# Optimization experiments

Measured on AMD Instinct MI355X. Metric: run time of the kernel, lower is better.

Reference implementation:

```python
import jax, jax.numpy as jnp
import numpy as np

BZ, IN_DIM, STATE_DIM, OUT_DIM, L = 16, 512, 512, 512, 2048
INIT_SCALE = 0.5


def setup_inputs() -> dict:
    key = jax.random.key(0)
    k_u, k_a, k_b, k_c = jax.random.split(key, 4)
    u = jax.random.normal(k_u, (BZ, IN_DIM, L), dtype=jnp.float32)
    A_unconstrained = jax.random.normal(k_a, (STATE_DIM,), dtype=jnp.float32) * 0.1
    B = jax.random.normal(k_b, (STATE_DIM, IN_DIM), dtype=jnp.float32) * INIT_SCALE / np.sqrt(IN_DIM)
    C = jax.random.normal(k_c, (OUT_DIM, STATE_DIM), dtype=jnp.float32) * INIT_SCALE / np.sqrt(STATE_DIM)
    D = jnp.zeros((OUT_DIM, IN_DIM), dtype=jnp.float32)
    h0 = jnp.zeros((STATE_DIM,), dtype=jnp.float32)
    return {"u": u, "A_unconstrained": A_unconstrained, "B": B, "C": C, "D": D, "h0": h0}


def reference(u, A_unconstrained, B, C, D, h0):
    # u: (Bz, input_dim, L)
    Bz = u.shape[0]
    A_diag = -jax.nn.softplus(A_unconstrained)  # (S,)
    # Time-invariant input projection, batched over all timesteps: (L, Bz, S)
    Bu = jnp.einsum('bil,si->lbs', u, B)

    state0 = jnp.broadcast_to(h0[None, :], (Bz, h0.shape[0]))

    def step(state, bu_t):
        x_t = state * A_diag[None, :] + bu_t  # (Bz, S)
        return x_t, x_t

    _, xs = jax.lax.scan(step, state0, Bu)  # xs: (L, Bz, S)

    # Output projection: y_t = C x_t + D u_t  -> (Bz, out, L)
    Y = jnp.einsum('lbs,os->bol', xs, C) + jnp.einsum('bil,oi->bol', u, D)
    return Y
```

## Files before the change

kernel.cpp:

```cpp
#include <hip/hip_runtime.h>
#include <math.h>

typedef __bf16 bf16;
typedef __bf16 bf16x2 __attribute__((ext_vector_type(2)));
typedef __bf16 bf16x4 __attribute__((ext_vector_type(4)));
typedef __bf16 bf16x8 __attribute__((ext_vector_type(8)));
typedef float  f32x4  __attribute__((ext_vector_type(4)));

#define BZd 16
#define INd 512
#define Sd  512
#define Od  512
#define Ld  2048
#define CLd 128
#define NCd (Ld / CLd)

__global__ __launch_bounds__(256) void prep_all(const float* __restrict__ B,
                                                const float* __restrict__ C,
                                                const float* __restrict__ D,
                                                const float* __restrict__ Au,
                                                bf16* __restrict__ Bb, bf16* __restrict__ Cb,
                                                bf16* __restrict__ Db, float* __restrict__ A_diag,
                                                int* __restrict__ dflag) {
    int bid = blockIdx.x;
    if (bid == 768) {
        #pragma unroll
        for (int r = 0; r < 2; ++r) {
            int ss = threadIdx.x + r * 256;
            float x = Au[ss];
            float sp = fmaxf(x, 0.0f) + log1pf(expf(-fabsf(x)));
            A_diag[ss] = -sp;
        }
        return;
    }
    int which = bid >> 8, lb = bid & 255;
    const float* src = which == 0 ? B : (which == 1 ? C : D);
    bf16* dst = which == 0 ? Bb : (which == 1 ? Cb : Db);
    int i = lb * 256 + threadIdx.x;
    float4 v = *(const float4*)&src[(size_t)i * 4];
    bf16x4 o = { (bf16)v.x, (bf16)v.y, (bf16)v.z, (bf16)v.w };
    *(bf16x4*)&dst[(size_t)i * 4] = o;
    if (which == 2) {
        bool nz = (v.x != 0.f) | (v.y != 0.f) | (v.z != 0.f) | (v.w != 0.f);
        unsigned long long bl = __ballot(nz);
        if (bl && ((threadIdx.x & 63) == 0)) atomicOr(dflag, 1);
    }
}

__global__ __launch_bounds__(256) void transp_u(const float* __restrict__ u,
                                                bf16* __restrict__ ut) {
    __shared__ bf16 t[64][73];
    int b = blockIdx.z, i0 = blockIdx.y * 64, l0 = blockIdx.x * 64;
    int tid = threadIdx.x, tx = tid & 15, ty = tid >> 4;
    const float* ub = u + ((size_t)b * INd + i0) * Ld + l0;
    #pragma unroll
    for (int r = 0; r < 4; ++r) {
        int il = r * 16 + ty;
        float4 v = *(const float4*)&ub[(size_t)il * Ld + tx * 4];
        t[il][tx * 4 + 0] = (bf16)v.x;
        t[il][tx * 4 + 1] = (bf16)v.y;
        t[il][tx * 4 + 2] = (bf16)v.z;
        t[il][tx * 4 + 3] = (bf16)v.w;
    }
    __syncthreads();
    bf16* uo = ut + ((size_t)b * Ld + l0) * INd + i0;
    #pragma unroll
    for (int it = 0; it < 2; ++it) {
        int q = it * 256 + tid;
        int lr = q >> 3;
        int ic = (q & 7) * 8;
        bf16x8 o;
        #pragma unroll
        for (int e = 0; e < 8; ++e) o[e] = t[ic + e][lr];
        *(bf16x8*)&uo[(size_t)lr * INd + ic] = o;
    }
}

template<bool OBF16>
__global__ __launch_bounds__(512, 2) void gemm8p(
    const bf16* __restrict__ A0, size_t aBS0,
    const bf16* __restrict__ B0, size_t bBS0,
    const bf16* __restrict__ A1, size_t aBS1,
    const bf16* __restrict__ B1, size_t bBS1,
    const int* __restrict__ dfp,
    void* __restrict__ OutV, size_t oBS, int ldOut,
    int NX, int NY)
{
    __shared__ bf16 lds[4 * 16384];
    const int tid = threadIdx.x;
    const int lane = tid & 63, w = tid >> 6;

    int nwg = gridDim.x, bid = blockIdx.x;
    int cpx = nwg >> 3;
    int swz = (bid & 7) * cpx + (bid >> 3);
    int pb = NX * NY;
    int b  = swz / pb;
    int r0 = swz - b * pb;
    int by = r0 / NX;
    int bx = r0 - by * NX;

    const int wm = w >> 2, wn = w & 3;
    const int fr = lane & 15, g = lane >> 4;

    int extra = dfp ? *dfp : 0;
    const int NT = extra ? 16 : 8;
    const int NU = 2 * NT;

    const bf16* Ab0 = A0 + (size_t)b * aBS0 + (size_t)(by * 256) * 512;
    const bf16* Bb0 = B0 + (size_t)b * bBS0 + (size_t)(bx * 256) * 512;
    const bf16* Ab1 = A1 + (size_t)b * aBS1 + (size_t)(by * 256) * 512;
    const bf16* Bb1 = B1 + (size_t)b * bBS1 + (size_t)(bx * 256) * 512;

    f32x4 acc[8][4];
    #pragma unroll
    for (int i = 0; i < 8; ++i)
        #pragma unroll
        for (int j = 0; j < 4; ++j)
            acc[i][j] = (f32x4){0.f, 0.f, 0.f, 0.f};

    auto stage_part = [&](int U, int isB) {
        int T = U >> 1, kh = U & 1;
        const bf16* Mb = isB ? (T >= 8 ? Bb1 : Bb0) : (T >= 8 ? Ab1 : Ab0);
        int kbase = ((T & 7) << 6) + (kh << 5);
        int slot = U & 3;
        #pragma unroll
        for (int rblk = 0; rblk < 2; ++rblk) {
            int row = rblk * 128 + (tid >> 2);
            int pos = tid & 3;
            int cs = pos ^ ((row & 3) ^ ((row >> 2) & 3));
            __builtin_amdgcn_global_load_lds(
                (const __attribute__((address_space(1))) void*)(Mb + (size_t)row * 512 + kbase + cs * 8),
                (__attribute__((address_space(3))) void*)&lds[slot * 16384 + isB * 8192 + (rblk * 128 + w * 16) * 32],
                16, 0, 0);
        }
    };

    stage_part(0, 0); stage_part(0, 1);
    stage_part(1, 0); stage_part(1, 1);
    stage_part(2, 0); stage_part(2, 1);

    bf16x8 av[4], bv[4];
    for (int U = 0; U < NU; ++U) {
        int ahead = NU - 1 - U;
        if (ahead >= 2)      { asm volatile("s_waitcnt vmcnt(8)" ::: "memory"); }
        else if (ahead == 1) { asm volatile("s_waitcnt vmcnt(4)" ::: "memory"); }
        else                 { asm volatile("s_waitcnt vmcnt(0)" ::: "memory"); }
        __builtin_amdgcn_sched_barrier(0);
        __builtin_amdgcn_s_barrier();
        __builtin_amdgcn_sched_barrier(0);

        const bf16* Ls = &lds[(U & 3) * 16384];
        #pragma unroll
        for (int mf = 0; mf < 2; ++mf) {
            if (mf == 1) {
                __builtin_amdgcn_sched_barrier(0);
                __builtin_amdgcn_s_barrier();
                __builtin_amdgcn_sched_barrier(0);
            }
            if (mf == 0) {
                #pragma unroll
                for (int j = 0; j < 4; ++j) {
                    int R = wn * 64 + j * 16 + fr;
                    int pos = g ^ ((R & 3) ^ ((R >> 2) & 3));
                    bv[j] = *(const bf16x8*)&Ls[8192 + R * 32 + pos * 8];
                }
            }
            #pragma unroll
            for (int i = 0; i < 4; ++i) {
                int R = wm * 128 + (mf * 4 + i) * 16 + fr;
                int pos = g ^ ((R & 3) ^ ((R >> 2) & 3));
                av[i] = *(const bf16x8*)&Ls[R * 32 + pos * 8];
            }
            if (U + 3 < NU) stage_part(U + 3, mf);
            asm volatile("s_waitcnt lgkmcnt(0)" ::: "memory");
            __builtin_amdgcn_sched_barrier(0);
            __builtin_amdgcn_s_setprio(1);
            #pragma unroll
            for (int i = 0; i < 4; ++i)
                #pragma unroll
                for (int j = 0; j < 4; ++j)
                    acc[mf * 4 + i][j] = __builtin_amdgcn_mfma_f32_16x16x32_bf16(
                        av[i], bv[j], acc[mf * 4 + i][j], 0, 0, 0);
            __builtin_amdgcn_s_setprio(0);
        }
    }

    int m0 = by * 256 + wm * 128 + g * 4;
    int n0 = bx * 256 + wn * 64 + fr;
    if (OBF16) {
        bf16* out = (bf16*)OutV + (size_t)b * oBS;
        #pragma unroll
        for (int i = 0; i < 8; ++i)
            #pragma unroll
            for (int j = 0; j < 4; ++j)
                #pragma unroll
                for (int q = 0; q < 4; ++q)
                    out[(size_t)(m0 + i * 16 + q) * ldOut + n0 + j * 16] = (bf16)acc[i][j][q];
    } else {
        float* out = (float*)OutV + (size_t)b * oBS;
        #pragma unroll
        for (int i = 0; i < 8; ++i)
            #pragma unroll
            for (int j = 0; j < 4; ++j)
                #pragma unroll
                for (int q = 0; q < 4; ++q)
                    out[(size_t)(m0 + i * 16 + q) * ldOut + n0 + j * 16] = acc[i][j][q];
    }
}

__global__ __launch_bounds__(256) void pass_ce2(const bf16* __restrict__ xbuf,
                                                const float* __restrict__ A_diag,
                                                float* __restrict__ ce) {
    int gI = blockIdx.x * 256 + threadIdx.x;
    int sp = gI & 255;
    int c = (gI >> 8) & (NCd - 1);
    int b = gI >> 12;
    int s = sp * 2;
    float a0 = A_diag[s], a1 = A_diag[s + 1];
    const bf16* p = xbuf + ((size_t)b * Ld + (size_t)c * CLd) * Sd + s;
    float x0 = 0.f, x1 = 0.f;
    #pragma unroll 4
    for (int j = 0; j < CLd; ++j) {
        bf16x2 v = *(const bf16x2*)&p[(size_t)j * Sd];
        x0 = fmaf(a0, x0, (float)v[0]);
        x1 = fmaf(a1, x1, (float)v[1]);
    }
    float2 o = { x0, x1 };
    *(float2*)&ce[((size_t)b * NCd + c) * Sd + s] = o;
}

__global__ __launch_bounds__(256) void pass_scan2(bf16* __restrict__ xbuf,
                                                  const float* __restrict__ A_diag,
                                                  const float* __restrict__ ce,
                                                  const float* __restrict__ h0) {
    int gI = blockIdx.x * 256 + threadIdx.x;
    int sp = gI & 255;
    int c = (gI >> 8) & (NCd - 1);
    int b = gI >> 12;
    int s = sp * 2;
    float a0 = A_diag[s], a1 = A_diag[s + 1];
    float acl0 = a0, acl1 = a1;
    #pragma unroll
    for (int i = 0; i < 7; ++i) { acl0 *= acl0; acl1 *= acl1; }
    float x0 = h0[s], x1 = h0[s + 1];
    for (int cp = 0; cp < NCd; ++cp) {
        if (cp >= c) break;
        float2 e = *(const float2*)&ce[((size_t)b * NCd + cp) * Sd + s];
        x0 = fmaf(acl0, x0, e.x);
        x1 = fmaf(acl1, x1, e.y);
    }
    bf16* p = xbuf + ((size_t)b * Ld + (size_t)c * CLd) * Sd + s;
    #pragma unroll 4
    for (int j = 0; j < CLd; ++j) {
        bf16x2 v = *(const bf16x2*)&p[(size_t)j * Sd];
        x0 = fmaf(a0, x0, (float)v[0]);
        x1 = fmaf(a1, x1, (float)v[1]);
        bf16x2 o = { (bf16)x0, (bf16)x1 };
        *(bf16x2*)&p[(size_t)j * Sd] = o;
    }
}

extern "C" void kernel_launch(void* const* d_in, const int* in_sizes, int n_in,
                              void* d_out, int out_size, void* d_ws, size_t ws_size,
                              hipStream_t stream) {
    const float* u  = (const float*)d_in[0];
    const float* Au = (const float*)d_in[1];
    const float* Bm = (const float*)d_in[2];
    const float* Cm = (const float*)d_in[3];
    const float* Dm = (const float*)d_in[4];
    const float* h0 = (const float*)d_in[5];
    float* Y = (float*)d_out;

    char* ws = (char*)d_ws;
    bf16* bu = (bf16*)ws;
    bf16* ut = (bf16*)(ws + (32ull << 20));
    bf16* Bb = (bf16*)(ws + (64ull << 20));
    bf16* Cb = Bb + 262144;
    bf16* Db = Cb + 262144;
    float* A_diag = (float*)(ws + (64ull << 20) + 3ull * 524288);
    float* ce   = A_diag + 512;
    int*   flag = (int*)(ce + (size_t)BZd * NCd * Sd);

    hipMemsetAsync(flag, 0, sizeof(int), stream);
    prep_all<<<769, 256, 0, stream>>>(Bm, Cm, Dm, Au, Bb, Cb, Db, A_diag, flag);
    transp_u<<<dim3(Ld / 64, INd / 64, BZd), 256, 0, stream>>>(u, ut);

    gemm8p<true><<<(Sd / 256) * (Ld / 256) * BZd, 512, 0, stream>>>(
        ut, (size_t)Ld * INd, Bb, 0,
        ut, (size_t)Ld * INd, Bb, 0,
        nullptr,
        (void*)bu, (size_t)Ld * Sd, Sd,
        Sd / 256, Ld / 256);

    pass_ce2<<<(BZd * NCd * (Sd / 2)) / 256, 256, 0, stream>>>(bu, A_diag, ce);
    pass_scan2<<<(BZd * NCd * (Sd / 2)) / 256, 256, 0, stream>>>(bu, A_diag, ce, h0);

    gemm8p<false><<<(Ld / 256) * (Od / 256) * BZd, 512, 0, stream>>>(
        Cb, 0, bu, (size_t)Ld * Sd,
        Db, 0, ut, (size_t)Ld * INd,
        flag,
        (void*)Y, (size_t)Od * Ld, Ld,
        Ld / 256, Od / 256);
}
```

Before: 108.1 us.

## Fuse chunk-end scan reduction into projection GEMM epilogue, drop flag memset

Computes each 128-step chunk's end state directly from the fp32 GEMM accumulators in the first GEMM's epilogue, using Horner evaluation with powers of A and cross-lane shuffles. This removes the separate pass_ce2 kernel and its full re-read of the bf16 Bu buffer. The D-nonzero flag becomes a per-block array written without atomics and is reduced by a wave vote inside the second GEMM, so the hipMemsetAsync launch goes away. In exchange the GEMM epilogue grows, and the chunk-end values now come from fp32 accumulators rather than the bf16-rounded Bu that the downstream scan reads.

```diff
diff --git a/kernel.cpp b/kernel.cpp
--- a/kernel.cpp
+++ b/kernel.cpp
@@ -21,7 +21,8 @@
                                                 const float* __restrict__ Au,
                                                 bf16* __restrict__ Bb, bf16* __restrict__ Cb,
                                                 bf16* __restrict__ Db, float* __restrict__ A_diag,
-                                                int* __restrict__ dflag) {
+                                                int* __restrict__ dfa) {
+    __shared__ int sred[4];
     int bid = blockIdx.x;
     if (bid == 768) {
         #pragma unroll
@@ -41,9 +42,12 @@
     bf16x4 o = { (bf16)v.x, (bf16)v.y, (bf16)v.z, (bf16)v.w };
     *(bf16x4*)&dst[(size_t)i * 4] = o;
     if (which == 2) {
-        bool nz = (v.x != 0.f) | (v.y != 0.f) | (v.z != 0.f) | (v.w != 0.f);
+        int nz = (v.x != 0.f) | (v.y != 0.f) | (v.z != 0.f) | (v.w != 0.f);
         unsigned long long bl = __ballot(nz);
-        if (bl && ((threadIdx.x & 63) == 0)) atomicOr(dflag, 1);
+        int wv = threadIdx.x >> 6;
+        if ((threadIdx.x & 63) == 0) sred[wv] = (bl != 0ull);
+        __syncthreads();
+        if (threadIdx.x == 0) dfa[lb] = sred[0] | sred[1] | sred[2] | sred[3];
     }
 }
 
@@ -82,7 +86,8 @@
     const bf16* __restrict__ B0, size_t bBS0,
     const bf16* __restrict__ A1, size_t aBS1,
     const bf16* __restrict__ B1, size_t bBS1,
-    const int* __restrict__ dfp,
+    const int* __restrict__ dfa,
+    const float* __restrict__ A_diag, float* __restrict__ cePtr,
     void* __restrict__ OutV, size_t oBS, int ldOut,
     int NX, int NY)
 {
@@ -102,7 +107,11 @@
     const int wm = w >> 2, wn = w & 3;
     const int fr = lane & 15, g = lane >> 4;
 
-    int extra = dfp ? *dfp : 0;
+    int extra = 0;
+    if (dfa) {
+        int4 f = ((const int4*)dfa)[lane];
+        extra = __any((f.x | f.y | f.z | f.w) != 0) ? 1 : 0;
+    }
     const int NT = extra ? 16 : 8;
     const int NU = 2 * NT;
 
@@ -185,6 +194,29 @@
         }
     }
 
+    if (OBF16 && cePtr) {
+        int colBase = bx * 256 + wn * 64;
+        #pragma unroll
+        for (int j = 0; j < 4; ++j) {
+            float a = A_diag[colBase + j * 16 + fr];
+            float a2 = a * a, a4 = a2 * a2, a8 = a4 * a4, a16 = a8 * a8;
+            float S = 0.f;
+            #pragma unroll
+            for (int I = 0; I < 8; ++I) {
+                f32x4 v = acc[I][j];
+                float e = fmaf(fmaf(fmaf(v[0], a, v[1]), a, v[2]), a, v[3]);
+                float e0 = __shfl(e, fr);
+                float e1 = __shfl(e, fr + 16);
+                float e2 = __shfl(e, fr + 32);
+                float e3 = __shfl(e, fr + 48);
+                float E = fmaf(fmaf(fmaf(e0, a4, e1), a4, e2), a4, e3);
+                S = fmaf(S, a16, E);
+            }
+            if (g == 0)
+                cePtr[((size_t)b * NCd + (by * 2 + wm)) * Sd + colBase + j * 16 + fr] = S;
+        }
+    }
+
     int m0 = by * 256 + wm * 128 + g * 4;
     int n0 = bx * 256 + wn * 64 + fr;
     if (OBF16) {
@@ -206,27 +238,6 @@
                 for (int q = 0; q < 4; ++q)
                     out[(size_t)(m0 + i * 16 + q) * ldOut + n0 + j * 16] = acc[i][j][q];
     }
-}
-
-__global__ __launch_bounds__(256) void pass_ce2(const bf16* __restrict__ xbuf,
-                                                const float* __restrict__ A_diag,
-                                                float* __restrict__ ce) {
-    int gI = blockIdx.x * 256 + threadIdx.x;
-    int sp = gI & 255;
-    int c = (gI >> 8) & (NCd - 1);
-    int b = gI >> 12;
-    int s = sp * 2;
-    float a0 = A_diag[s], a1 = A_diag[s + 1];
-    const bf16* p = xbuf + ((size_t)b * Ld + (size_t)c * CLd) * Sd + s;
-    float x0 = 0.f, x1 = 0.f;
-    #pragma unroll 4
-    for (int j = 0; j < CLd; ++j) {
-        bf16x2 v = *(const bf16x2*)&p[(size_t)j * Sd];
-        x0 = fmaf(a0, x0, (float)v[0]);
-        x1 = fmaf(a1, x1, (float)v[1]);
-    }
-    float2 o = { x0, x1 };
-    *(float2*)&ce[((size_t)b * NCd + c) * Sd + s] = o;
 }
 
 __global__ __launch_bounds__(256) void pass_scan2(bf16* __restrict__ xbuf,
@@ -279,26 +290,26 @@
     bf16* Db = Cb + 262144;
     float* A_diag = (float*)(ws + (64ull << 20) + 3ull * 524288);
     float* ce   = A_diag + 512;
-    int*   flag = (int*)(ce + (size_t)BZd * NCd * Sd);
-
-    hipMemsetAsync(flag, 0, sizeof(int), stream);
-    prep_all<<<769, 256, 0, stream>>>(Bm, Cm, Dm, Au, Bb, Cb, Db, A_diag, flag);
+    int*   dfa  = (int*)(ce + (size_t)BZd * NCd * Sd);
+
+    prep_all<<<769, 256, 0, stream>>>(Bm, Cm, Dm, Au, Bb, Cb, Db, A_diag, dfa);
     transp_u<<<dim3(Ld / 64, INd / 64, BZd), 256, 0, stream>>>(u, ut);
 
     gemm8p<true><<<(Sd / 256) * (Ld / 256) * BZd, 512, 0, stream>>>(
         ut, (size_t)Ld * INd, Bb, 0,
         ut, (size_t)Ld * INd, Bb, 0,
         nullptr,
+        A_diag, ce,
         (void*)bu, (size_t)Ld * Sd, Sd,
         Sd / 256, Ld / 256);
 
-    pass_ce2<<<(BZd * NCd * (Sd / 2)) / 256, 256, 0, stream>>>(bu, A_diag, ce);
     pass_scan2<<<(BZd * NCd * (Sd / 2)) / 256, 256, 0, stream>>>(bu, A_diag, ce, h0);
 
     gemm8p<false><<<(Ld / 256) * (Od / 256) * BZd, 512, 0, stream>>>(
         Cb, 0, bu, (size_t)Ld * Sd,
         Db, 0, ut, (size_t)Ld * INd,
-        flag,
+        dfa,
+        A_diag, nullptr,
         (void*)Y, (size_t)Od * Ld, Ld,
         Ld / 256, Od / 256);
 }
```

Result: faster. 97.25 us (-10.1%).
